# Kernel tuning notes

Hardware: AMD Instinct MI355X
Metric: run time of the kernel (lower is better)

Reference implementation:

```python
import jax, jax.numpy as jnp
import numpy as np

MASK_VALUE = -1e6  # torch code uses -1000000.0, not -inf


def setup_inputs() -> dict:
    key = jax.random.key(0)
    k1, k2, k3, k4 = jax.random.split(key, 4)
    B, Nq, Nk, d = 32, 2048, 2048, 128
    return {
        "querys": jax.random.normal(k1, (B, Nq, d), dtype=jnp.float32),
        "keys": jax.random.normal(k2, (B, Nk, d), dtype=jnp.float32),
        "values": jax.random.normal(k3, (B, Nk, d), dtype=jnp.float32),
        "valid_seq_len": jax.random.randint(k4, (B,), 1, Nk + 1, dtype=jnp.int32),
    }


def reference(querys, keys, values, valid_seq_len):
    # querys: [B, Nq, d], keys/values: [B, Nk, d], valid_seq_len: [B]
    d = querys.shape[-1]
    scale = 1.0 / jnp.sqrt(jnp.asarray(d, dtype=querys.dtype))
    # scores: [B, Nq, Nk]
    scores = jnp.einsum("bqd,bkd->bqk", querys, keys) * scale
    Nk = keys.shape[1]
    # mask key positions >= valid length (per batch, broadcast over queries)
    mask = jnp.arange(Nk, dtype=jnp.int32)[None, None, :] < valid_seq_len[:, None, None]
    scores = jnp.where(mask, scores, jnp.asarray(MASK_VALUE, dtype=scores.dtype))
    attn = jax.nn.softmax(scores, axis=-1)
    # dropout prob = 0.0 -> identity
    out = jnp.einsum("bqk,bkd->bqd", attn, values)
    return out
```

## Files before the change

kernel.cpp:

```cpp
#include <hip/hip_runtime.h>
#include <cstdint>
#include <math.h>

typedef unsigned short ushort_t;
typedef unsigned int uint_t;
typedef __bf16 v8bf __attribute__((ext_vector_type(8)));
typedef float v16f __attribute__((ext_vector_type(16)));

constexpr int B_SZ = 32, NQ = 2048, NK = 2048, DH = 128;
constexpr int BK = 64;
constexpr int TILE_E = 8192;
constexpr float QSCALE = 0.12751880226116815f;
constexpr float M2 = 17.312340490667561f;

__device__ __forceinline__ float4 ld4f(const float* p) {
  return *reinterpret_cast<const float4*>(p);
}
__device__ __forceinline__ uint4 ld4u(const ushort_t* p) {
  return *reinterpret_cast<const uint4*>(p);
}

__device__ inline v8bf cvt8(const float* __restrict__ p) {
  float4 f0 = ld4f(p);
  float4 f1 = ld4f(p + 4);
  v8bf r;
  r[0] = (__bf16)f0.x; r[1] = (__bf16)f0.y; r[2] = (__bf16)f0.z; r[3] = (__bf16)f0.w;
  r[4] = (__bf16)f1.x; r[5] = (__bf16)f1.y; r[6] = (__bf16)f1.z; r[7] = (__bf16)f1.w;
  return r;
}

__device__ inline v8bf cvt8s(const float* __restrict__ p, float s) {
  float4 f0 = ld4f(p);
  float4 f1 = ld4f(p + 4);
  v8bf r;
  r[0] = (__bf16)(f0.x * s); r[1] = (__bf16)(f0.y * s);
  r[2] = (__bf16)(f0.z * s); r[3] = (__bf16)(f0.w * s);
  r[4] = (__bf16)(f1.x * s); r[5] = (__bf16)(f1.y * s);
  r[6] = (__bf16)(f1.z * s); r[7] = (__bf16)(f1.w * s);
  return r;
}

__device__ __forceinline__ uint_t pk2(float a, float b) {
  const ushort_t ua = __builtin_bit_cast(ushort_t, (__bf16)a);
  const ushort_t ub = __builtin_bit_cast(ushort_t, (__bf16)b);
  return (uint_t)ua | ((uint_t)ub << 16);
}

__global__ __launch_bounds__(256) void prep_k(const float* __restrict__ K,
                                              ushort_t* __restrict__ Kf) {
  const int b = blockIdx.y, tq = blockIdx.x, t = threadIdx.x;
  const int l32 = t & 31, g = t >> 5;
  const float* Kb = K + ((size_t)(b * NK + tq * 64)) * DH;
  ushort_t* out = Kf + ((size_t)(b * 32 + tq)) * TILE_E;
  for (int c = 0; c < 4; ++c) {
    const int id = g * 4 + c;
    const int kb = id >> 4, ks = (id >> 1) & 7, hi = id & 1;
    v8bf v = cvt8(Kb + (size_t)(kb * 32 + l32) * DH + (2 * ks + hi) * 8);
    *reinterpret_cast<v8bf*>(out + (size_t)id * 256 + l32 * 8) = v;
  }
}

__global__ __launch_bounds__(256) void prep_v(const float* __restrict__ V,
                                              ushort_t* __restrict__ Vf) {
  __shared__ __align__(16) ushort_t st[64 * 128];
  const int b = blockIdx.y, tq = blockIdx.x, k0 = tq * 64, t = threadIdx.x;
  for (int c = 0; c < 4; ++c) {
    const int row = (t >> 4) + 16 * c;
    const int col = (t & 15) * 8;
    v8bf v = cvt8(V + ((size_t)(b * NK + k0 + row)) * DH + col);
    const int chunk = (col >> 3) ^ ((row >> 3) & 7);
    *reinterpret_cast<v8bf*>(&st[row * 128 + chunk * 8]) = v;
  }
  __syncthreads();
  ushort_t* out = Vf + ((size_t)(b * 32 + tq)) * TILE_E;
  const int l32 = t & 31, f0 = t >> 5;
  for (int c = 0; c < 4; ++c) {
    const int f = f0 + 8 * c;
    const int nb = f & 3, hi = (f >> 2) & 1, ksg = f >> 3;
    const int d = nb * 32 + l32;
    alignas(16) ushort_t tmp[8];
    for (int j = 0; j < 8; ++j) {
      const int row = ksg * 16 + hi * 8 + j;
      const int elem = (d & 7) | (((d >> 3) ^ ((row >> 3) & 7)) << 3);
      tmp[j] = st[row * 128 + elem];
    }
    *reinterpret_cast<uint4*>(out + ((ksg * 2 + hi) * 4 + nb) * 256 + l32 * 8) =
        *reinterpret_cast<const uint4*>(tmp);
  }
}

__device__ __forceinline__ void qk_sm(const ushort_t* kt, int l32, int hi, int k0n,
                                      int valid, const v8bf* qf, float& ls0,
                                      float& ls1, uint4& pa0, uint4& pa1,
                                      uint4& pa2, uint4& pa3) {
  const bool part = (k0n + BK > valid);
#pragma unroll
  for (int kb = 0; kb < 2; ++kb) {
    const ushort_t* base = kt + kb * 4096 + hi * 256 + l32 * 8;
    const uint4 kf0 = ld4u(base + 0 * 512);
    const uint4 kf1 = ld4u(base + 1 * 512);
    const uint4 kf2 = ld4u(base + 2 * 512);
    const uint4 kf3 = ld4u(base + 3 * 512);
    const uint4 kf4 = ld4u(base + 4 * 512);
    const uint4 kf5 = ld4u(base + 5 * 512);
    const uint4 kf6 = ld4u(base + 6 * 512);
    const uint4 kf7 = ld4u(base + 7 * 512);
    v16f sa;
#pragma unroll
    for (int r = 0; r < 16; ++r) sa[r] = 0.f;
    __builtin_amdgcn_s_setprio(1);
    sa = __builtin_amdgcn_mfma_f32_32x32x16_bf16(__builtin_bit_cast(v8bf, kf0), qf[0], sa, 0, 0, 0);
    sa = __builtin_amdgcn_mfma_f32_32x32x16_bf16(__builtin_bit_cast(v8bf, kf1), qf[1], sa, 0, 0, 0);
    sa = __builtin_amdgcn_mfma_f32_32x32x16_bf16(__builtin_bit_cast(v8bf, kf2), qf[2], sa, 0, 0, 0);
    sa = __builtin_amdgcn_mfma_f32_32x32x16_bf16(__builtin_bit_cast(v8bf, kf3), qf[3], sa, 0, 0, 0);
    sa = __builtin_amdgcn_mfma_f32_32x32x16_bf16(__builtin_bit_cast(v8bf, kf4), qf[4], sa, 0, 0, 0);
    sa = __builtin_amdgcn_mfma_f32_32x32x16_bf16(__builtin_bit_cast(v8bf, kf5), qf[5], sa, 0, 0, 0);
    sa = __builtin_amdgcn_mfma_f32_32x32x16_bf16(__builtin_bit_cast(v8bf, kf6), qf[6], sa, 0, 0, 0);
    sa = __builtin_amdgcn_mfma_f32_32x32x16_bf16(__builtin_bit_cast(v8bf, kf7), qf[7], sa, 0, 0, 0);
    __builtin_amdgcn_s_setprio(0);
    float p[16];
#pragma unroll
    for (int r = 0; r < 16; ++r) {
      const int crow = (r & 3) + 8 * (r >> 2) + 4 * hi;
      float x = sa[r];
      if (part) x = (k0n + kb * 32 + crow < valid) ? x : -1e30f;
      float e;
      asm("v_exp_f32 %0, %1" : "=v"(e) : "v"(x - M2));
      p[r] = e;
      if (r < 8) ls0 += e; else ls1 += e;
    }
#pragma unroll
    for (int q2 = 0; q2 < 2; ++q2) {
      uint_t A0 = pk2(p[8 * q2 + 0], p[8 * q2 + 1]);
      uint_t A1 = pk2(p[8 * q2 + 2], p[8 * q2 + 3]);
      uint_t B0 = pk2(p[8 * q2 + 4], p[8 * q2 + 5]);
      uint_t B1 = pk2(p[8 * q2 + 6], p[8 * q2 + 7]);
      asm("v_permlane32_swap_b32 %0, %1" : "+v"(A0), "+v"(B0));
      asm("v_permlane32_swap_b32 %0, %1" : "+v"(A1), "+v"(B1));
      uint4 fw;
      fw.x = A0; fw.y = A1; fw.z = B0; fw.w = B1;
      if (kb == 0) { if (q2 == 0) pa0 = fw; else pa1 = fw; }
      else         { if (q2 == 0) pa2 = fw; else pa3 = fw; }
    }
  }
}

__device__ __forceinline__ void pv4(const ushort_t* vt, int l32, int hi,
                                    const uint4 paf, int ksg, v16f* o) {
  const ushort_t* vb = vt + ksg * 2048 + hi * 1024 + l32 * 8;
  const uint4 vf0 = ld4u(vb + 0 * 256);
  const uint4 vf1 = ld4u(vb + 1 * 256);
  const uint4 vf2 = ld4u(vb + 2 * 256);
  const uint4 vf3 = ld4u(vb + 3 * 256);
  const v8bf pa = __builtin_bit_cast(v8bf, paf);
  __builtin_amdgcn_s_setprio(1);
  o[0] = __builtin_amdgcn_mfma_f32_32x32x16_bf16(pa, __builtin_bit_cast(v8bf, vf0), o[0], 0, 0, 0);
  o[1] = __builtin_amdgcn_mfma_f32_32x32x16_bf16(pa, __builtin_bit_cast(v8bf, vf1), o[1], 0, 0, 0);
  o[2] = __builtin_amdgcn_mfma_f32_32x32x16_bf16(pa, __builtin_bit_cast(v8bf, vf2), o[2], 0, 0, 0);
  o[3] = __builtin_amdgcn_mfma_f32_32x32x16_bf16(pa, __builtin_bit_cast(v8bf, vf3), o[3], 0, 0, 0);
  __builtin_amdgcn_s_setprio(0);
}

__global__ __launch_bounds__(256, 2) void attn(const float* __restrict__ Q,
                                               const ushort_t* __restrict__ Kf,
                                               const ushort_t* __restrict__ Vf,
                                               const int* __restrict__ vsl,
                                               float* __restrict__ Out) {
  __shared__ int s_ord[32];
  __shared__ float mO[2][4096];
  __shared__ float sRS[2][32];

  const int t = threadIdx.x;
  const int lane = t & 63, w = t >> 6;
  const int wq = w & 1, pr = w >> 1;
  const int hi = lane >> 5, l32 = lane & 31;

  if (t < 32) {
    const int cx = (vsl[t] + 63) >> 6;
    int rank = 0;
    for (int y = 0; y < 32; ++y) {
      const int cy = (vsl[y] + 63) >> 6;
      rank += (cy > cx) || (cy == cx && y < t);
    }
    s_ord[rank] = t;
  }
  __syncthreads();
  const int n = (int)blockIdx.x;
  const int ci = n & 255, cj = n >> 8;
  const int rk = (cj == 0) ? ci : (cj == 1) ? 511 - ci : (cj == 2) ? 512 + ci : 1023 - ci;
  const int b = s_ord[rk >> 5];
  const int qt = rk & 31;

  const int q0 = qt * 64;
  const int valid = vsl[b];
  const int nt = (valid + BK - 1) / BK;
  const int myNt = (nt + 1 - pr) >> 1;

  v8bf qf[8];
  {
    const float* qp = Q + ((size_t)(b * NQ + q0 + wq * 32 + l32)) * DH + hi * 8;
#pragma unroll
    for (int ks = 0; ks < 8; ++ks) qf[ks] = cvt8s(qp + ks * 16, QSCALE);
  }

  v16f o[4];
#pragma unroll
  for (int nb = 0; nb < 4; ++nb)
#pragma unroll
    for (int r = 0; r < 16; ++r) o[nb][r] = 0.f;
  float ls0 = 0.f, ls1 = 0.f;

  const ushort_t* Kb = Kf + (size_t)b * 32 * TILE_E;
  const ushort_t* Vb = Vf + (size_t)b * 32 * TILE_E;

  for (int i = 0; i < myNt; ++i) {
    const int tile = 2 * i + pr;
    const ushort_t* kt = Kb + (size_t)tile * TILE_E;
    const ushort_t* vt = Vb + (size_t)tile * TILE_E;
    uint4 pa0, pa1, pa2, pa3;
    qk_sm(kt, l32, hi, tile * BK, valid, qf, ls0, ls1, pa0, pa1, pa2, pa3);
    pv4(vt, l32, hi, pa0, 0, o);
    pv4(vt, l32, hi, pa1, 1, o);
    pv4(vt, l32, hi, pa2, 2, o);
    pv4(vt, l32, hi, pa3, 3, o);
  }

  const float lsw = ls0 + ls1;
  const float rsw = lsw + __shfl_xor(lsw, 32);
  if (pr == 1) {
#pragma unroll
    for (int nb = 0; nb < 4; ++nb)
#pragma unroll
      for (int r = 0; r < 16; ++r)
        mO[wq][(nb * 16 + r) * 64 + lane] = o[nb][r];
    if (hi == 0) sRS[wq][l32] = rsw;
  }
  __syncthreads();
  if (pr == 0) {
    const float rs = rsw + sRS[wq][l32];
#pragma unroll
    for (int nb = 0; nb < 4; ++nb)
#pragma unroll
      for (int r = 0; r < 16; ++r) o[nb][r] += mO[wq][(nb * 16 + r) * 64 + lane];
    const float inv_own = 1.0f / rs;
#pragma unroll
    for (int r = 0; r < 16; ++r) {
      const int crow = (r & 3) + 8 * (r >> 2) + 4 * hi;
      const float inv = __shfl(inv_own, crow);
      float* op = Out + ((size_t)(b * NQ + q0 + wq * 32 + crow)) * DH + l32;
#pragma unroll
      for (int nb = 0; nb < 4; ++nb) op[nb * 32] = o[nb][r] * inv;
    }
  }
}

extern "C" void kernel_launch(void* const* d_in, const int* in_sizes, int n_in,
                              void* d_out, int out_size, void* d_ws, size_t ws_size,
                              hipStream_t stream) {
  const float* Q = (const float*)d_in[0];
  const float* K = (const float*)d_in[1];
  const float* V = (const float*)d_in[2];
  const int* vsl = (const int*)d_in[3];
  float* Out = (float*)d_out;

  ushort_t* Kf = (ushort_t*)d_ws;
  ushort_t* Vf = Kf + (size_t)B_SZ * 32 * TILE_E;

  prep_k<<<dim3(NK / 64, B_SZ), dim3(256), 0, stream>>>(K, Kf);
  prep_v<<<dim3(NK / 64, B_SZ), dim3(256), 0, stream>>>(V, Vf);
  attn<<<dim3(1024), dim3(256), 0, stream>>>(Q, Kf, Vf, vsl, Out);
}
```

Measured before the change: 198.7 us.

## Split KV across four waves per 32-query block and fuse K/V prep kernels

The attention kernel now assigns 32 query rows per block and splits the key tiles across all four waves, reducing partial results through shared memory in a two-level tree. The grid doubles to 2048 blocks to improve load balance across variable valid lengths. The separate K and V conversion kernels are merged into one launch. The trade-off is halved K/V reuse per block, so more K/V traffic, plus extra barriers in the reduction.

```diff
diff --git a/kernel.cpp b/kernel.cpp
--- a/kernel.cpp
+++ b/kernel.cpp
@@ -46,24 +46,23 @@
   return (uint_t)ua | ((uint_t)ub << 16);
 }
 
-__global__ __launch_bounds__(256) void prep_k(const float* __restrict__ K,
-                                              ushort_t* __restrict__ Kf) {
-  const int b = blockIdx.y, tq = blockIdx.x, t = threadIdx.x;
-  const int l32 = t & 31, g = t >> 5;
-  const float* Kb = K + ((size_t)(b * NK + tq * 64)) * DH;
-  ushort_t* out = Kf + ((size_t)(b * 32 + tq)) * TILE_E;
-  for (int c = 0; c < 4; ++c) {
-    const int id = g * 4 + c;
-    const int kb = id >> 4, ks = (id >> 1) & 7, hi = id & 1;
-    v8bf v = cvt8(Kb + (size_t)(kb * 32 + l32) * DH + (2 * ks + hi) * 8);
-    *reinterpret_cast<v8bf*>(out + (size_t)id * 256 + l32 * 8) = v;
-  }
-}
-
-__global__ __launch_bounds__(256) void prep_v(const float* __restrict__ V,
-                                              ushort_t* __restrict__ Vf) {
+__global__ __launch_bounds__(256) void prep_kv(const float* __restrict__ K,
+                                               const float* __restrict__ V,
+                                               ushort_t* __restrict__ Kf,
+                                               ushort_t* __restrict__ Vf) {
   __shared__ __align__(16) ushort_t st[64 * 128];
   const int b = blockIdx.y, tq = blockIdx.x, k0 = tq * 64, t = threadIdx.x;
+  const int l32 = t & 31, g = t >> 5;
+  {
+    const float* Kb = K + ((size_t)(b * NK + k0)) * DH;
+    ushort_t* out = Kf + ((size_t)(b * 32 + tq)) * TILE_E;
+    for (int c = 0; c < 4; ++c) {
+      const int id = g * 4 + c;
+      const int kb = id >> 4, ks = (id >> 1) & 7, hi = id & 1;
+      v8bf v = cvt8(Kb + (size_t)(kb * 32 + l32) * DH + (2 * ks + hi) * 8);
+      *reinterpret_cast<v8bf*>(out + (size_t)id * 256 + l32 * 8) = v;
+    }
+  }
   for (int c = 0; c < 4; ++c) {
     const int row = (t >> 4) + 16 * c;
     const int col = (t & 15) * 8;
@@ -72,20 +71,21 @@
     *reinterpret_cast<v8bf*>(&st[row * 128 + chunk * 8]) = v;
   }
   __syncthreads();
-  ushort_t* out = Vf + ((size_t)(b * 32 + tq)) * TILE_E;
-  const int l32 = t & 31, f0 = t >> 5;
-  for (int c = 0; c < 4; ++c) {
-    const int f = f0 + 8 * c;
-    const int nb = f & 3, hi = (f >> 2) & 1, ksg = f >> 3;
-    const int d = nb * 32 + l32;
-    alignas(16) ushort_t tmp[8];
-    for (int j = 0; j < 8; ++j) {
-      const int row = ksg * 16 + hi * 8 + j;
-      const int elem = (d & 7) | (((d >> 3) ^ ((row >> 3) & 7)) << 3);
-      tmp[j] = st[row * 128 + elem];
-    }
-    *reinterpret_cast<uint4*>(out + ((ksg * 2 + hi) * 4 + nb) * 256 + l32 * 8) =
-        *reinterpret_cast<const uint4*>(tmp);
+  {
+    ushort_t* out = Vf + ((size_t)(b * 32 + tq)) * TILE_E;
+    for (int c = 0; c < 4; ++c) {
+      const int f = g + 8 * c;
+      const int nb = f & 3, hi = (f >> 2) & 1, ksg = f >> 3;
+      const int d = nb * 32 + l32;
+      alignas(16) ushort_t tmp[8];
+      for (int j = 0; j < 8; ++j) {
+        const int row = ksg * 16 + hi * 8 + j;
+        const int elem = (d & 7) | (((d >> 3) ^ ((row >> 3) & 7)) << 3);
+        tmp[j] = st[row * 128 + elem];
+      }
+      *reinterpret_cast<uint4*>(out + ((ksg * 2 + hi) * 4 + nb) * 256 + l32 * 8) =
+          *reinterpret_cast<const uint4*>(tmp);
+    }
   }
 }
 
@@ -167,12 +167,11 @@
                                                const int* __restrict__ vsl,
                                                float* __restrict__ Out) {
   __shared__ int s_ord[32];
-  __shared__ float mO[2][4096];
   __shared__ float sRS[2][32];
+  __shared__ __align__(16) float mO[2][4096];
 
   const int t = threadIdx.x;
   const int lane = t & 63, w = t >> 6;
-  const int wq = w & 1, pr = w >> 1;
   const int hi = lane >> 5, l32 = lane & 31;
 
   if (t < 32) {
@@ -187,18 +186,18 @@
   __syncthreads();
   const int n = (int)blockIdx.x;
   const int ci = n & 255, cj = n >> 8;
-  const int rk = (cj == 0) ? ci : (cj == 1) ? 511 - ci : (cj == 2) ? 512 + ci : 1023 - ci;
-  const int b = s_ord[rk >> 5];
-  const int qt = rk & 31;
-
-  const int q0 = qt * 64;
+  const int rk = cj * 256 + ((cj & 1) ? 255 - ci : ci);
+  const int b = s_ord[rk >> 6];
+  const int qt = rk & 63;
+
+  const int q0 = qt * 32;
   const int valid = vsl[b];
   const int nt = (valid + BK - 1) / BK;
-  const int myNt = (nt + 1 - pr) >> 1;
+  const int myNt = (nt > w) ? ((nt - w + 3) >> 2) : 0;
 
   v8bf qf[8];
   {
-    const float* qp = Q + ((size_t)(b * NQ + q0 + wq * 32 + l32)) * DH + hi * 8;
+    const float* qp = Q + ((size_t)(b * NQ + q0 + l32)) * DH + hi * 8;
 #pragma unroll
     for (int ks = 0; ks < 8; ++ks) qf[ks] = cvt8s(qp + ks * 16, QSCALE);
   }
@@ -214,7 +213,7 @@
   const ushort_t* Vb = Vf + (size_t)b * 32 * TILE_E;
 
   for (int i = 0; i < myNt; ++i) {
-    const int tile = 2 * i + pr;
+    const int tile = 4 * i + w;
     const ushort_t* kt = Kb + (size_t)tile * TILE_E;
     const ushort_t* vt = Vb + (size_t)tile * TILE_E;
     uint4 pa0, pa1, pa2, pa3;
@@ -226,28 +225,45 @@
   }
 
   const float lsw = ls0 + ls1;
-  const float rsw = lsw + __shfl_xor(lsw, 32);
-  if (pr == 1) {
-#pragma unroll
-    for (int nb = 0; nb < 4; ++nb)
-#pragma unroll
-      for (int r = 0; r < 16; ++r)
-        mO[wq][(nb * 16 + r) * 64 + lane] = o[nb][r];
-    if (hi == 0) sRS[wq][l32] = rsw;
-  }
-  __syncthreads();
-  if (pr == 0) {
-    const float rs = rsw + sRS[wq][l32];
-#pragma unroll
-    for (int nb = 0; nb < 4; ++nb)
-#pragma unroll
-      for (int r = 0; r < 16; ++r) o[nb][r] += mO[wq][(nb * 16 + r) * 64 + lane];
+  float rsw = lsw + __shfl_xor(lsw, 32);
+  if (w == 1 || w == 3) {
+    const int s = w >> 1;
+#pragma unroll
+    for (int nb = 0; nb < 4; ++nb)
+#pragma unroll
+      for (int r = 0; r < 16; ++r) mO[s][(nb * 16 + r) * 64 + lane] = o[nb][r];
+    if (hi == 0) sRS[s][l32] = rsw;
+  }
+  __syncthreads();
+  if (w == 0 || w == 2) {
+    const int s = w >> 1;
+#pragma unroll
+    for (int nb = 0; nb < 4; ++nb)
+#pragma unroll
+      for (int r = 0; r < 16; ++r) o[nb][r] += mO[s][(nb * 16 + r) * 64 + lane];
+    rsw += sRS[s][l32];
+  }
+  __syncthreads();
+  if (w == 2) {
+#pragma unroll
+    for (int nb = 0; nb < 4; ++nb)
+#pragma unroll
+      for (int r = 0; r < 16; ++r) mO[0][(nb * 16 + r) * 64 + lane] = o[nb][r];
+    if (hi == 0) sRS[0][l32] = rsw;
+  }
+  __syncthreads();
+  if (w == 0) {
+#pragma unroll
+    for (int nb = 0; nb < 4; ++nb)
+#pragma unroll
+      for (int r = 0; r < 16; ++r) o[nb][r] += mO[0][(nb * 16 + r) * 64 + lane];
+    const float rs = rsw + sRS[0][l32];
     const float inv_own = 1.0f / rs;
 #pragma unroll
     for (int r = 0; r < 16; ++r) {
       const int crow = (r & 3) + 8 * (r >> 2) + 4 * hi;
       const float inv = __shfl(inv_own, crow);
-      float* op = Out + ((size_t)(b * NQ + q0 + wq * 32 + crow)) * DH + l32;
+      float* op = Out + ((size_t)(b * NQ + q0 + crow)) * DH + l32;
 #pragma unroll
       for (int nb = 0; nb < 4; ++nb) op[nb * 32] = o[nb][r] * inv;
     }
@@ -266,7 +282,6 @@
   ushort_t* Kf = (ushort_t*)d_ws;
   ushort_t* Vf = Kf + (size_t)B_SZ * 32 * TILE_E;
 
-  prep_k<<<dim3(NK / 64, B_SZ), dim3(256), 0, stream>>>(K, Kf);
-  prep_v<<<dim3(NK / 64, B_SZ), dim3(256), 0, stream>>>(V, Vf);
-  attn<<<dim3(1024), dim3(256), 0, stream>>>(Q, Kf, Vf, vsl, Out);
-}
+  prep_kv<<<dim3(NK / 64, B_SZ), dim3(256), 0, stream>>>(K, V, Kf, Vf);
+  attn<<<dim3(2048), dim3(256), 0, stream>>>(Q, Kf, Vf, vsl, Out);
+}
```

Result: slower. 208.4 us (+4.9%).
